# Kernel tuning notes

Hardware: AMD Instinct MI355X
Metric: run time of the kernel (lower is better)

Reference implementation:

```python
import jax, jax.numpy as jnp
import numpy as np
import math

B, D, C = 2048, 512, 10572


def setup_inputs() -> dict:
    key = jax.random.key(0)
    k1, k2, k3 = jax.random.split(key, 3)
    feat = jax.random.normal(k1, (B, D), dtype=jnp.float32)
    label = jax.random.randint(k2, (B,), 0, C, dtype=jnp.int64)
    # xavier-uniform init for the class weight matrix [C, D]
    limit = math.sqrt(6.0 / (C + D))
    weights = jax.random.uniform(k3, (C, D), dtype=jnp.float32, minval=-limit, maxval=limit)
    return {"feat": feat, "label": label, "weights": weights}


def reference(feat, label, weights):
    class_num = weights.shape[0]
    scale = math.sqrt(2.0) * math.log(class_num - 1)  # auto-scale init, overrides ctor arg
    pi = math.pi

    # L2-normalize features and class weights, cosine similarity logits
    nf = feat / jnp.linalg.norm(feat, axis=-1, keepdims=True)
    nw = weights / jnp.linalg.norm(weights, axis=-1, keepdims=True)
    cos = jnp.matmul(nf, nw.T)          # [B, C]
    logits = scale * cos                 # [B, C]
    probs = jax.nn.softmax(logits, axis=-1)  # detached in original

    idx = jnp.arange(cos.shape[0])
    cos_gt = cos[idx, label]             # [B] cosine at ground-truth class
    logit_gt = logits[idx, label]
    p_gt = probs[idx, label]

    theta = jnp.arccos(cos_gt)           # radians
    thetas_deg = theta / pi * 180.0
    B_vals = jnp.exp(logit_gt) * (1.0 / p_gt - 1.0)

    # clamp angle to < pi/2 before margin rescale
    d_theta = jnp.where(theta >= pi / 2.0, pi / 2.0 - 0.01, theta)
    s = (1.0 / cos_gt) * jnp.log(B_vals * (pi / (2.0 * d_theta) - 1.0))
    s = jax.lax.stop_gradient(s)         # s built from .data/.numpy() (detached) in torch

    # scatter per-sample rescaled logit back at the ground-truth column
    new_logits = logits.at[idx, label].set(s * cos_gt)

    avg_p = jnp.mean(p_gt)
    min_p = jnp.min(p_gt)
    max_p = jnp.max(p_gt)
    B_avg = jnp.arccos(jnp.log(jnp.mean(B_vals) / (class_num - 1)) / scale) / pi * 180.0
    # (thetas stats are printed only in the original; avg kept implicit)
    _ = (jnp.min(thetas_deg), jnp.max(thetas_deg), jnp.mean(thetas_deg))

    return (cos, new_logits, avg_p, min_p, max_p, B_avg, 0, 0)
```

## Files before the change

kernel.cpp:

```cpp
#include <hip/hip_runtime.h>
#include <hip/hip_bf16.h>
#include <cmath>

#define B_ROWS 2048
#define D_DIM 512
#define C_COLS 10572
#define WPAD 10624

#define BM 128
#define BN 128
#define BK 32
#define NSTEP (D_DIM / BK)

typedef __attribute__((ext_vector_type(8))) short short8;
typedef __attribute__((ext_vector_type(4))) float f32x4;

__device__ __host__ inline int swz(int a) { return a ^ (((a >> 7) & 7) << 4); }

__device__ inline void load_lds16(const void* g, const void* l) {
    __builtin_amdgcn_global_load_lds(
        (const __attribute__((address_space(1))) unsigned int*)g,
        (__attribute__((address_space(3))) unsigned int*)l, 16, 0, 0);
}

__global__ __launch_bounds__(256) void normcast_kernel(
    const float* __restrict__ feat, const float* __restrict__ wts,
    __hip_bfloat16* __restrict__ fhi, __hip_bfloat16* __restrict__ whi,
    float* __restrict__ rowsum) {
    int idx = blockIdx.x * 4 + (threadIdx.x >> 6);
    int lane = threadIdx.x & 63;
    const float* src;
    __hip_bfloat16* dst;
    if (idx < B_ROWS) {
        src = feat + (size_t)idx * D_DIM;
        dst = fhi + (size_t)idx * D_DIM;
        if (lane == 0) rowsum[idx] = 0.0f;
    } else {
        int r = idx - B_ROWS;
        dst = whi + (size_t)r * D_DIM;
        if (r >= C_COLS) {
            short8 z = {0, 0, 0, 0, 0, 0, 0, 0};
            *(short8*)(dst + lane * 8) = z;
            return;
        }
        src = wts + (size_t)r * D_DIM;
    }
    float4 a = *(const float4*)(src + lane * 8);
    float4 b = *(const float4*)(src + lane * 8 + 4);
    float ss = a.x * a.x + a.y * a.y + a.z * a.z + a.w * a.w +
               b.x * b.x + b.y * b.y + b.z * b.z + b.w * b.w;
#pragma unroll
    for (int off = 32; off > 0; off >>= 1) ss += __shfl_xor(ss, off);
    float rn = 1.0f / sqrtf(ss);
    float v[8] = {a.x * rn, a.y * rn, a.z * rn, a.w * rn,
                  b.x * rn, b.y * rn, b.z * rn, b.w * rn};
    short8 o;
#pragma unroll
    for (int k = 0; k < 8; ++k) {
        __hip_bfloat16 h = __float2bfloat16(v[k]);
        o[k] = *reinterpret_cast<short*>(&h);
    }
    *(short8*)(dst + lane * 8) = o;
}

__global__ __launch_bounds__(256) void gemm_bf16_kernel(
    const __hip_bfloat16* __restrict__ fhi, const __hip_bfloat16* __restrict__ whi,
    float* __restrict__ cosm, float* __restrict__ logits, float* __restrict__ rowsum,
    float scale) {
    __shared__ __align__(16) char smem[49152];

    int tid = threadIdx.x;
    int lane = tid & 63;
    int w = tid >> 6;
    int wr = w >> 1, wc = w & 1;

    int orig = blockIdx.y * gridDim.x + blockIdx.x;
    int s = (orig & 7) * 166 + (orig >> 3);
    int by = s & 15;
    int bx = s >> 4;
    int row0 = by * BM;
    int col0 = bx * BN;

    int grow[2], gcol[2], ldsw[2];
#pragma unroll
    for (int i = 0; i < 2; ++i) {
        int o = i * 4096 + tid * 16;
        int q = swz(o);
        grow[i] = q >> 6;
        gcol[i] = (q & 63) >> 1;
        ldsw[i] = i * 4096 + w * 1024;
    }

    int r = lane & 15, kb = lane >> 4;
    int aoff[4], boff[4];
#pragma unroll
    for (int m = 0; m < 4; ++m) {
        aoff[m] = swz((wr * 64 + m * 16 + r) * 64 + kb * 16);
        boff[m] = swz((wc * 64 + m * 16 + r) * 64 + kb * 16);
    }

    const __hip_bfloat16* Ap = fhi + (size_t)row0 * D_DIM;
    const __hip_bfloat16* Bp = whi + (size_t)col0 * D_DIM;

    auto stage = [&](int k0, int b) {
#pragma unroll
        for (int i = 0; i < 2; ++i) {
            size_t go = (size_t)grow[i] * D_DIM + k0 + gcol[i];
            load_lds16(Ap + go, smem + b * 8192 + ldsw[i]);
            load_lds16(Bp + go, smem + 24576 + b * 8192 + ldsw[i]);
        }
    };

    f32x4 acc[4][4] = {};

    stage(0, 0);
    stage(BK, 1);
    asm volatile("s_waitcnt vmcnt(4)" ::: "memory");
    __builtin_amdgcn_s_barrier();
    __builtin_amdgcn_sched_barrier(0);

    int cur = 0, sb = 2;
    for (int t = 0; t < NSTEP; ++t) {
        if (t + 2 < NSTEP) stage((t + 2) * BK, sb);
        const char* Ab = smem + cur * 8192;
        const char* Bb = smem + 24576 + cur * 8192;
        short8 af[4], bf[4];
#pragma unroll
        for (int m = 0; m < 4; ++m) af[m] = *(const short8*)(Ab + aoff[m]);
#pragma unroll
        for (int n = 0; n < 4; ++n) bf[n] = *(const short8*)(Bb + boff[n]);
        __builtin_amdgcn_s_setprio(1);
#pragma unroll
        for (int m = 0; m < 4; ++m)
#pragma unroll
            for (int n = 0; n < 4; ++n)
                acc[m][n] = __builtin_amdgcn_mfma_f32_16x16x32_bf16(af[m], bf[n],
                                                                    acc[m][n], 0, 0, 0);
        __builtin_amdgcn_s_setprio(0);
        if (t + 2 < NSTEP)
            asm volatile("s_waitcnt vmcnt(4)" ::: "memory");
        else
            asm volatile("s_waitcnt vmcnt(0)" ::: "memory");
        __builtin_amdgcn_s_barrier();
        __builtin_amdgcn_sched_barrier(0);
        cur = (cur == 2) ? 0 : cur + 1;
        sb = (sb == 2) ? 0 : sb + 1;
    }

    float* tl = (float*)smem;
    const int LROW = 132;
    int trow8 = tid >> 5;
    int c4 = tid & 31;
    bool cvalid = (col0 + c4 * 4) < C_COLS;

#pragma unroll
    for (int half = 0; half < 2; ++half) {
        if (wr == half) {
#pragma unroll
            for (int m = 0; m < 4; ++m)
#pragma unroll
                for (int n = 0; n < 4; ++n) {
                    int lc = wc * 64 + n * 16 + (lane & 15);
#pragma unroll
                    for (int j = 0; j < 4; ++j) {
                        int lr = m * 16 + (lane >> 4) * 4 + j;
                        tl[lr * LROW + lc] = acc[m][n][j];
                    }
                }
        }
        __syncthreads();
#pragma unroll
        for (int it = 0; it < 8; ++it) {
            int lrow = it * 8 + trow8;
            int orow = row0 + half * 64 + lrow;
            float se = 0.f;
            float4 v = *(const float4*)&tl[lrow * LROW + c4 * 4];
            if (cvalid) {
                size_t o = (size_t)orow * C_COLS + col0 + c4 * 4;
                *(float4*)&cosm[o] = v;
                float4 lg = make_float4(scale * v.x, scale * v.y, scale * v.z,
                                        scale * v.w);
                *(float4*)&logits[o] = lg;
                se = __expf(lg.x) + __expf(lg.y) + __expf(lg.z) + __expf(lg.w);
            }
#pragma unroll
            for (int off = 1; off < 32; off <<= 1) se += __shfl_xor(se, off);
            if (c4 == 0) atomicAdd(&rowsum[orow], se);
        }
        __syncthreads();
    }
}

__global__ __launch_bounds__(256) void gt_fix_kernel(
    const float* __restrict__ feat, const float* __restrict__ weights,
    const int* __restrict__ label, const float* __restrict__ rowsum,
    float* __restrict__ cosm, float* __restrict__ logits,
    float* __restrict__ pgt, float* __restrict__ bvals, float scale) {
    int row = blockIdx.x * 4 + (threadIdx.x >> 6);
    int lane = threadIdx.x & 63;
    if (row >= B_ROWS) return;
    int lbl = label[row];
    const float4* f4 = (const float4*)(feat + (size_t)row * D_DIM);
    const float4* w4 = (const float4*)(weights + (size_t)lbl * D_DIM);
    float ff = 0.f, ww = 0.f, fw = 0.f;
#pragma unroll
    for (int i = 0; i < 2; ++i) {
        float4 a = f4[lane + i * 64];
        float4 b = w4[lane + i * 64];
        ff += a.x * a.x + a.y * a.y + a.z * a.z + a.w * a.w;
        ww += b.x * b.x + b.y * b.y + b.z * b.z + b.w * b.w;
        fw += a.x * b.x + a.y * b.y + a.z * b.z + a.w * b.w;
    }
#pragma unroll
    for (int off = 32; off > 0; off >>= 1) {
        ff += __shfl_xor(ff, off);
        ww += __shfl_xor(ww, off);
        fw += __shfl_xor(fw, off);
    }
    if (lane == 0) {
        float cg = fw / (sqrtf(ff) * sqrtf(ww));
        float S = rowsum[row];
        float e = expf(scale * cg);
        float p = e / S;
        float Bv = S - e;
        const float PI = 3.14159265358979323846f;
        float marg;
        if (cg > 0.f) {
            marg = asinf(cg) / acosf(cg);
        } else {
            float dth = 0.5f * PI - 0.01f;
            marg = PI / (2.0f * dth) - 1.0f;
        }
        size_t o = (size_t)row * C_COLS + lbl;
        cosm[o] = cg;
        logits[o] = logf(Bv * marg);
        pgt[row] = p;
        bvals[row] = Bv;
    }
}

__global__ __launch_bounds__(256) void finalize_kernel(const float* __restrict__ pgt,
                                                       const float* __restrict__ bvals,
                                                       float* __restrict__ tail,
                                                       float scale) {
    int tid = threadIdx.x;
    float s = 0.f, mn = 1e30f, mx = -1e30f, sb = 0.f;
    for (int i = tid; i < B_ROWS; i += 256) {
        float p = pgt[i];
        s += p;
        mn = fminf(mn, p);
        mx = fmaxf(mx, p);
        sb += bvals[i];
    }
#pragma unroll
    for (int off = 32; off > 0; off >>= 1) {
        s += __shfl_down(s, off);
        mn = fminf(mn, __shfl_down(mn, off));
        mx = fmaxf(mx, __shfl_down(mx, off));
        sb += __shfl_down(sb, off);
    }
    __shared__ float rs[4], rmn[4], rmx[4], rsb[4];
    int wave = tid >> 6;
    if ((tid & 63) == 0) { rs[wave] = s; rmn[wave] = mn; rmx[wave] = mx; rsb[wave] = sb; }
    __syncthreads();
    if (tid == 0) {
        float S = 0.f, MN = 1e30f, MX = -1e30f, SB = 0.f;
        for (int ww = 0; ww < 4; ++ww) {
            S += rs[ww]; MN = fminf(MN, rmn[ww]); MX = fmaxf(MX, rmx[ww]); SB += rsb[ww];
        }
        const float PI = 3.14159265358979323846f;
        tail[0] = S / (float)B_ROWS;
        tail[1] = MN;
        tail[2] = MX;
        float meanB = SB / (float)B_ROWS;
        tail[3] = acosf(logf(meanB / (float)(C_COLS - 1)) / scale) / PI * 180.0f;
        tail[4] = 0.0f;
        tail[5] = 0.0f;
    }
}

extern "C" void kernel_launch(void* const* d_in, const int* in_sizes, int n_in,
                              void* d_out, int out_size, void* d_ws, size_t ws_size,
                              hipStream_t stream) {
    const float* feat = (const float*)d_in[0];
    const int* label = (const int*)d_in[1];
    const float* weights = (const float*)d_in[2];

    float* out = (float*)d_out;
    float* cos_out = out;
    float* logits_out = out + (size_t)B_ROWS * C_COLS;
    float* tail = out + (size_t)2 * B_ROWS * C_COLS;

    double scale_d = std::sqrt(2.0) * std::log((double)(C_COLS - 1));
    float scale = (float)scale_d;

    const size_t fsz = (size_t)B_ROWS * D_DIM * sizeof(__hip_bfloat16);
    const size_t wsz = (size_t)WPAD * D_DIM * sizeof(__hip_bfloat16);
    char* wsb = (char*)d_ws;
    __hip_bfloat16* fhi = (__hip_bfloat16*)wsb;
    __hip_bfloat16* whi = (__hip_bfloat16*)(wsb + fsz);
    float* rowsum = (float*)(wsb + fsz + wsz);
    float* pgt = rowsum + B_ROWS;
    float* bv = pgt + B_ROWS;

    normcast_kernel<<<(B_ROWS + WPAD) / 4, 256, 0, stream>>>(feat, weights, fhi, whi,
                                                             rowsum);

    dim3 grid(WPAD / BN, B_ROWS / BM);
    gemm_bf16_kernel<<<grid, 256, 0, stream>>>(fhi, whi, cos_out, logits_out, rowsum,
                                               scale);

    gt_fix_kernel<<<B_ROWS / 4, 256, 0, stream>>>(feat, weights, label, rowsum, cos_out,
                                                  logits_out, pgt, bv, scale);
    finalize_kernel<<<1, 256, 0, stream>>>(pgt, bv, tail, scale);
}
```

Measured before the change: 72.42 us.

## Process two row tiles per block and overlap first tile's epilogue with second GEMM

Each block now computes two vertically adjacent 128x128 output tiles in sequence, with the grid halved to 664 blocks. The K-loop pipeline runs continuously across both tiles. The first tile's results are written straight from registers to global memory, along with logits and row-sum atomics, interleaved with the second tile's MFMA steps. The aim is to hide output-store latency behind compute and cut the epilogue's exposed time. The cost is doubled accumulator registers, which may reduce occupancy, and uncoalesced scalar stores for the first tile.

```diff
diff --git a/kernel.cpp b/kernel.cpp
--- a/kernel.cpp
+++ b/kernel.cpp
@@ -74,20 +74,22 @@
     int w = tid >> 6;
     int wr = w >> 1, wc = w & 1;
 
-    int orig = blockIdx.y * gridDim.x + blockIdx.x;
-    int s = (orig & 7) * 166 + (orig >> 3);
-    int by = s & 15;
-    int bx = s >> 4;
-    int row0 = by * BM;
+    int orig = blockIdx.x;
+    int q = (orig & 7) * 83 + (orig >> 3);
+    int s0 = 2 * q;
+    int by0 = s0 & 15;
+    int bx = s0 >> 4;
+    int row0a = by0 * BM;
+    int row0b = row0a + BM;
     int col0 = bx * BN;
 
     int grow[2], gcol[2], ldsw[2];
 #pragma unroll
     for (int i = 0; i < 2; ++i) {
         int o = i * 4096 + tid * 16;
-        int q = swz(o);
-        grow[i] = q >> 6;
-        gcol[i] = (q & 63) >> 1;
+        int qq = swz(o);
+        grow[i] = qq >> 6;
+        gcol[i] = (qq & 63) >> 1;
         ldsw[i] = i * 4096 + w * 1024;
     }
 
@@ -99,29 +101,32 @@
         boff[m] = swz((wc * 64 + m * 16 + r) * 64 + kb * 16);
     }
 
-    const __hip_bfloat16* Ap = fhi + (size_t)row0 * D_DIM;
+    const __hip_bfloat16* Ap1 = fhi + (size_t)row0a * D_DIM;
+    const __hip_bfloat16* Ap2 = fhi + (size_t)row0b * D_DIM;
     const __hip_bfloat16* Bp = whi + (size_t)col0 * D_DIM;
 
-    auto stage = [&](int k0, int b) {
+    auto stage = [&](const __hip_bfloat16* Asrc, int k0, int b) {
 #pragma unroll
         for (int i = 0; i < 2; ++i) {
             size_t go = (size_t)grow[i] * D_DIM + k0 + gcol[i];
-            load_lds16(Ap + go, smem + b * 8192 + ldsw[i]);
+            load_lds16(Asrc + go, smem + b * 8192 + ldsw[i]);
             load_lds16(Bp + go, smem + 24576 + b * 8192 + ldsw[i]);
         }
     };
 
-    f32x4 acc[4][4] = {};
-
-    stage(0, 0);
-    stage(BK, 1);
+    f32x4 acc1[4][4] = {};
+    f32x4 acc2[4][4] = {};
+
+    stage(Ap1, 0, 0);
+    stage(Ap1, BK, 1);
     asm volatile("s_waitcnt vmcnt(4)" ::: "memory");
     __builtin_amdgcn_s_barrier();
     __builtin_amdgcn_sched_barrier(0);
 
     int cur = 0, sb = 2;
     for (int t = 0; t < NSTEP; ++t) {
-        if (t + 2 < NSTEP) stage((t + 2) * BK, sb);
+        int gs = t + 2;
+        stage(gs < 16 ? Ap1 : Ap2, (gs & 15) * BK, sb);
         const char* Ab = smem + cur * 8192;
         const char* Bb = smem + 24576 + cur * 8192;
         short8 af[4], bf[4];
@@ -134,11 +139,60 @@
         for (int m = 0; m < 4; ++m)
 #pragma unroll
             for (int n = 0; n < 4; ++n)
-                acc[m][n] = __builtin_amdgcn_mfma_f32_16x16x32_bf16(af[m], bf[n],
-                                                                    acc[m][n], 0, 0, 0);
+                acc1[m][n] = __builtin_amdgcn_mfma_f32_16x16x32_bf16(af[m], bf[n],
+                                                                     acc1[m][n], 0, 0, 0);
         __builtin_amdgcn_s_setprio(0);
-        if (t + 2 < NSTEP)
-            asm volatile("s_waitcnt vmcnt(4)" ::: "memory");
+        asm volatile("s_waitcnt vmcnt(4)" ::: "memory");
+        __builtin_amdgcn_s_barrier();
+        __builtin_amdgcn_sched_barrier(0);
+        cur = (cur == 2) ? 0 : cur + 1;
+        sb = (sb == 2) ? 0 : sb + 1;
+    }
+
+    cur = 1;
+    sb = 0;
+#pragma unroll
+    for (int t = 16; t < 32; ++t) {
+        if (t + 2 < 32) stage(Ap2, ((t + 2) & 15) * BK, sb);
+        const char* Ab = smem + cur * 8192;
+        const char* Bb = smem + 24576 + cur * 8192;
+        short8 af[4], bf[4];
+#pragma unroll
+        for (int m = 0; m < 4; ++m) af[m] = *(const short8*)(Ab + aoff[m]);
+#pragma unroll
+        for (int n = 0; n < 4; ++n) bf[n] = *(const short8*)(Bb + boff[n]);
+        __builtin_amdgcn_s_setprio(1);
+#pragma unroll
+        for (int m = 0; m < 4; ++m)
+#pragma unroll
+            for (int n = 0; n < 4; ++n)
+                acc2[m][n] = __builtin_amdgcn_mfma_f32_16x16x32_bf16(af[m], bf[n],
+                                                                     acc2[m][n], 0, 0, 0);
+        __builtin_amdgcn_s_setprio(0);
+
+        {
+            const int f = t - 16;
+            const int fm = f >> 2, fj = f & 3;
+            int rrow = row0a + wr * 64 + fm * 16 + (lane >> 4) * 4 + fj;
+            float se = 0.f;
+#pragma unroll
+            for (int n = 0; n < 4; ++n) {
+                int ccol = col0 + wc * 64 + n * 16 + (lane & 15);
+                float v = acc1[fm][n][fj];
+                if (ccol < C_COLS) {
+                    size_t o = (size_t)rrow * C_COLS + ccol;
+                    cosm[o] = v;
+                    logits[o] = scale * v;
+                    se += __expf(scale * v);
+                }
+            }
+#pragma unroll
+            for (int off = 1; off < 16; off <<= 1) se += __shfl_xor(se, off);
+            if ((lane & 15) == 0) atomicAdd(&rowsum[rrow], se);
+        }
+
+        if (t + 2 < 32)
+            asm volatile("s_waitcnt vmcnt(12)" ::: "memory");
         else
             asm volatile("s_waitcnt vmcnt(0)" ::: "memory");
         __builtin_amdgcn_s_barrier();
@@ -164,7 +218,7 @@
 #pragma unroll
                     for (int j = 0; j < 4; ++j) {
                         int lr = m * 16 + (lane >> 4) * 4 + j;
-                        tl[lr * LROW + lc] = acc[m][n][j];
+                        tl[lr * LROW + lc] = acc2[m][n][j];
                     }
                 }
         }
@@ -172,7 +226,7 @@
 #pragma unroll
         for (int it = 0; it < 8; ++it) {
             int lrow = it * 8 + trow8;
-            int orow = row0 + half * 64 + lrow;
+            int orow = row0b + half * 64 + lrow;
             float se = 0.f;
             float4 v = *(const float4*)&tl[lrow * LROW + c4 * 4];
             if (cvalid) {
@@ -306,9 +360,8 @@
     normcast_kernel<<<(B_ROWS + WPAD) / 4, 256, 0, stream>>>(feat, weights, fhi, whi,
                                                              rowsum);
 
-    dim3 grid(WPAD / BN, B_ROWS / BM);
-    gemm_bf16_kernel<<<grid, 256, 0, stream>>>(fhi, whi, cos_out, logits_out, rowsum,
-                                               scale);
+    gemm_bf16_kernel<<<664, 256, 0, stream>>>(fhi, whi, cos_out, logits_out, rowsum,
+                                              scale);
 
     gt_fix_kernel<<<B_ROWS / 4, 256, 0, stream>>>(feat, weights, label, rowsum, cos_out,
                                                   logits_out, pgt, bv, scale);
```

Result: slower. 80.64 us (+11.3%).

## Fold ground-truth cosine into prep kernel and merge gt fix with finalize

Applied to the files above, without the earlier changes.

The fp32 ground-truth cosine dot product now runs as extra blocks of the normalize/cast kernel before the GEMM. The per-row scatter of the rescaled logit and the final statistics reduction are merged into a single one-block kernel. This goes from four launches to three and removes the pgt/bvals round trip through memory. In exchange, the scatter of 2048 rows and its transcendental math now run serially in one 256-thread block instead of spread across 512 blocks.

```diff
diff --git a/kernel.cpp b/kernel.cpp
--- a/kernel.cpp
+++ b/kernel.cpp
@@ -12,6 +12,9 @@
 #define BK 32
 #define NSTEP (D_DIM / BK)
 
+#define NC_BLOCKS ((B_ROWS + WPAD) / 4)
+#define GT_BLOCKS (B_ROWS / 4)
+
 typedef __attribute__((ext_vector_type(8))) short short8;
 typedef __attribute__((ext_vector_type(4))) float f32x4;
 
@@ -23,12 +26,39 @@
         (__attribute__((address_space(3))) unsigned int*)l, 16, 0, 0);
 }
 
-__global__ __launch_bounds__(256) void normcast_kernel(
+__global__ __launch_bounds__(256) void prep_kernel(
     const float* __restrict__ feat, const float* __restrict__ wts,
+    const int* __restrict__ label,
     __hip_bfloat16* __restrict__ fhi, __hip_bfloat16* __restrict__ whi,
-    float* __restrict__ rowsum) {
-    int idx = blockIdx.x * 4 + (threadIdx.x >> 6);
+    float* __restrict__ rowsum, float* __restrict__ cge) {
+    int wave = threadIdx.x >> 6;
     int lane = threadIdx.x & 63;
+
+    if (blockIdx.x >= NC_BLOCKS) {
+        int row = (blockIdx.x - NC_BLOCKS) * 4 + wave;
+        int lbl = label[row];
+        const float4* f4 = (const float4*)(feat + (size_t)row * D_DIM);
+        const float4* w4 = (const float4*)(wts + (size_t)lbl * D_DIM);
+        float ff = 0.f, ww = 0.f, fw = 0.f;
+#pragma unroll
+        for (int i = 0; i < 2; ++i) {
+            float4 a = f4[lane + i * 64];
+            float4 b = w4[lane + i * 64];
+            ff += a.x * a.x + a.y * a.y + a.z * a.z + a.w * a.w;
+            ww += b.x * b.x + b.y * b.y + b.z * b.z + b.w * b.w;
+            fw += a.x * b.x + a.y * b.y + a.z * b.z + a.w * b.w;
+        }
+#pragma unroll
+        for (int off = 32; off > 0; off >>= 1) {
+            ff += __shfl_xor(ff, off);
+            ww += __shfl_xor(ww, off);
+            fw += __shfl_xor(fw, off);
+        }
+        if (lane == 0) cge[row] = fw / (sqrtf(ff) * sqrtf(ww));
+        return;
+    }
+
+    int idx = blockIdx.x * 4 + wave;
     const float* src;
     __hip_bfloat16* dst;
     if (idx < B_ROWS) {
@@ -191,39 +221,20 @@
     }
 }
 
-__global__ __launch_bounds__(256) void gt_fix_kernel(
-    const float* __restrict__ feat, const float* __restrict__ weights,
+__global__ __launch_bounds__(256) void gt_finalize_kernel(
     const int* __restrict__ label, const float* __restrict__ rowsum,
-    float* __restrict__ cosm, float* __restrict__ logits,
-    float* __restrict__ pgt, float* __restrict__ bvals, float scale) {
-    int row = blockIdx.x * 4 + (threadIdx.x >> 6);
-    int lane = threadIdx.x & 63;
-    if (row >= B_ROWS) return;
-    int lbl = label[row];
-    const float4* f4 = (const float4*)(feat + (size_t)row * D_DIM);
-    const float4* w4 = (const float4*)(weights + (size_t)lbl * D_DIM);
-    float ff = 0.f, ww = 0.f, fw = 0.f;
-#pragma unroll
-    for (int i = 0; i < 2; ++i) {
-        float4 a = f4[lane + i * 64];
-        float4 b = w4[lane + i * 64];
-        ff += a.x * a.x + a.y * a.y + a.z * a.z + a.w * a.w;
-        ww += b.x * b.x + b.y * b.y + b.z * b.z + b.w * b.w;
-        fw += a.x * b.x + a.y * b.y + a.z * b.z + a.w * b.w;
-    }
-#pragma unroll
-    for (int off = 32; off > 0; off >>= 1) {
-        ff += __shfl_xor(ff, off);
-        ww += __shfl_xor(ww, off);
-        fw += __shfl_xor(fw, off);
-    }
-    if (lane == 0) {
-        float cg = fw / (sqrtf(ff) * sqrtf(ww));
+    const float* __restrict__ cge, float* __restrict__ cosm,
+    float* __restrict__ logits, float* __restrict__ tail, float scale) {
+    int tid = threadIdx.x;
+    const float PI = 3.14159265358979323846f;
+    float s = 0.f, mn = 1e30f, mx = -1e30f, sb = 0.f;
+    for (int row = tid; row < B_ROWS; row += 256) {
+        int lbl = label[row];
+        float cg = cge[row];
         float S = rowsum[row];
         float e = expf(scale * cg);
         float p = e / S;
         float Bv = S - e;
-        const float PI = 3.14159265358979323846f;
         float marg;
         if (cg > 0.f) {
             marg = asinf(cg) / acosf(cg);
@@ -234,23 +245,10 @@
         size_t o = (size_t)row * C_COLS + lbl;
         cosm[o] = cg;
         logits[o] = logf(Bv * marg);
-        pgt[row] = p;
-        bvals[row] = Bv;
-    }
-}
-
-__global__ __launch_bounds__(256) void finalize_kernel(const float* __restrict__ pgt,
-                                                       const float* __restrict__ bvals,
-                                                       float* __restrict__ tail,
-                                                       float scale) {
-    int tid = threadIdx.x;
-    float s = 0.f, mn = 1e30f, mx = -1e30f, sb = 0.f;
-    for (int i = tid; i < B_ROWS; i += 256) {
-        float p = pgt[i];
         s += p;
         mn = fminf(mn, p);
         mx = fmaxf(mx, p);
-        sb += bvals[i];
+        sb += Bv;
     }
 #pragma unroll
     for (int off = 32; off > 0; off >>= 1) {
@@ -268,7 +266,6 @@
         for (int ww = 0; ww < 4; ++ww) {
             S += rs[ww]; MN = fminf(MN, rmn[ww]); MX = fmaxf(MX, rmx[ww]); SB += rsb[ww];
         }
-        const float PI = 3.14159265358979323846f;
         tail[0] = S / (float)B_ROWS;
         tail[1] = MN;
         tail[2] = MX;
@@ -300,17 +297,15 @@
     __hip_bfloat16* fhi = (__hip_bfloat16*)wsb;
     __hip_bfloat16* whi = (__hip_bfloat16*)(wsb + fsz);
     float* rowsum = (float*)(wsb + fsz + wsz);
-    float* pgt = rowsum + B_ROWS;
-    float* bv = pgt + B_ROWS;
-
-    normcast_kernel<<<(B_ROWS + WPAD) / 4, 256, 0, stream>>>(feat, weights, fhi, whi,
-                                                             rowsum);
+    float* cge = rowsum + B_ROWS;
+
+    prep_kernel<<<NC_BLOCKS + GT_BLOCKS, 256, 0, stream>>>(feat, weights, label, fhi,
+                                                           whi, rowsum, cge);
 
     dim3 grid(WPAD / BN, B_ROWS / BM);
     gemm_bf16_kernel<<<grid, 256, 0, stream>>>(fhi, whi, cos_out, logits_out, rowsum,
                                                scale);
 
-    gt_fix_kernel<<<B_ROWS / 4, 256, 0, stream>>>(feat, weights, label, rowsum, cos_out,
-                                                  logits_out, pgt, bv, scale);
-    finalize_kernel<<<1, 256, 0, stream>>>(pgt, bv, tail, scale);
-}
+    gt_finalize_kernel<<<1, 256, 0, stream>>>(label, rowsum, cge, cos_out, logits_out,
+                                              tail, scale);
+}
```

Measured after the change: 73.26 us. No clear change (+1.2%).
